# Performance work log

Hardware: AMD Instinct MI355X
Metric: run time of the kernel (lower is better)

Reference implementation:

```python
import jax, jax.numpy as jnp
import numpy as np

LATENT, U_DIM, NUM_PROD, NUM_INJ, FEAT_C = 128, 30, 20, 10, 128
WELL_IN = LATENT + U_DIM + FEAT_C  # 286
HID = 64
B = 16384


def setup_inputs() -> dict:
    key = jax.random.key(0)
    ks = jax.random.split(key, 12)
    s = lambda fan_in: 1.0 / np.sqrt(fan_in)
    return {
        "zt": jax.random.normal(ks[0], (B, LATENT), jnp.float32),
        "dt": 1,
        "ut": jax.random.normal(ks[1], (B, U_DIM), jnp.float32),
        "well_features": jax.random.normal(ks[2], (B, NUM_PROD, FEAT_C), jnp.float32),
        # StructuredODEFunc params: dz/dt = -(L L^T) z + Bm u
        "L": jax.random.normal(ks[3], (LATENT, LATENT), jnp.float32) * s(LATENT),
        "Bm": jax.random.normal(ks[4], (LATENT, U_DIM), jnp.float32) * s(U_DIM),
        # per-well MLP heads, stacked: [P, in, out]
        "W1": jax.random.uniform(ks[5], (NUM_PROD, WELL_IN, HID), jnp.float32, -s(WELL_IN), s(WELL_IN)),
        "b1": jax.random.uniform(ks[6], (NUM_PROD, HID), jnp.float32, -s(WELL_IN), s(WELL_IN)),
        "W2": jax.random.uniform(ks[7], (NUM_PROD, HID, 2), jnp.float32, -s(HID), s(HID)),
        "b2": jax.random.uniform(ks[8], (NUM_PROD, 2), jnp.float32, -s(HID), s(HID)),
        # injector head: Linear(latent+u_dim, num_inj)
        "Wi": jax.random.uniform(ks[9], (LATENT + U_DIM, NUM_INJ), jnp.float32, -s(LATENT + U_DIM), s(LATENT + U_DIM)),
        "bi": jax.random.uniform(ks[10], (NUM_INJ,), jnp.float32, -s(LATENT + U_DIM), s(LATENT + U_DIM)),
    }


def reference(zt, dt, ut, well_features, L, Bm, W1, b1, W2, b2, Wi, bi):
    # ODE step: A = -L L^T, f(z) = A z + Bm u; euler over t_span [0,1] -> one step h=1
    A = -(L @ L.T)                                  # [D, D]
    zt1 = zt + zt @ A.T + ut @ Bm.T                 # [B, D]
    zu = jnp.concatenate([zt1, ut], axis=-1)        # [B, D+U]
    # per-well heads, fused as batched gather-MLP
    zu_b = jnp.broadcast_to(zu[:, None, :], (zu.shape[0], NUM_PROD, zu.shape[1]))
    head_in = jnp.concatenate([zu_b, well_features], axis=-1)        # [B, P, WELL_IN]
    h = jax.nn.relu(jnp.einsum('bpi,pih->bph', head_in, W1) + b1)    # [B, P, 64]
    well_out = jnp.einsum('bph,pho->bpo', h, W2) + b2                # [B, P, 2]
    well_out = well_out.reshape(well_out.shape[0], NUM_PROD * 2)     # concat order matches loop
    inj_out = zu @ Wi + bi                                           # [B, num_inj]
    yt1 = jnp.concatenate([well_out, inj_out], axis=-1)              # [B, 2P+I]
    return zt1, yt1
```

## Files before the change

kernel.cpp:

```cpp
#include <hip/hip_runtime.h>

#define BATCH   16384
#define LATENT  128
#define U_DIM   30
#define NUM_PROD 20
#define NUM_INJ 10
#define FEAT_C  128
#define WELL_IN 286
#define HID     64
#define ZT1_N   (BATCH*LATENT)
#define OUT_ROW (NUM_PROD*2+NUM_INJ)

typedef unsigned short u16;
typedef __attribute__((ext_vector_type(8))) short  short8;
typedef __attribute__((ext_vector_type(4))) float  floatx4;

__device__ __forceinline__ u16 f2bf(float f){
    unsigned x = __builtin_bit_cast(unsigned, f);
    x += 0x7fffu + ((x >> 16) & 1u);
    return (u16)(x >> 16);
}
__device__ __forceinline__ short8 cvt8(floatx4 a, floatx4 b){
    short8 s;
    s[0]=(short)f2bf(a[0]); s[1]=(short)f2bf(a[1]);
    s[2]=(short)f2bf(a[2]); s[3]=(short)f2bf(a[3]);
    s[4]=(short)f2bf(b[0]); s[5]=(short)f2bf(b[1]);
    s[6]=(short)f2bf(b[2]); s[7]=(short)f2bf(b[3]);
    return s;
}

#define NW1  368640
#define NGS  20480
#define NWIS 2560
#define NW2S 20480
__device__ u16 g_w1s[NW1];
__device__ u16 g_gs [NGS];
__device__ u16 g_wis[NWIS];
__device__ u16 g_w2s[NW2S];

__global__ __launch_bounds__(256) void prep_kernel(
    const float* __restrict__ L, const float* __restrict__ Bm,
    const float* __restrict__ W1, const float* __restrict__ Wi,
    const float* __restrict__ W2)
{
    const int bx = blockIdx.x, t = threadIdx.x;
    if (bx < 180) {
        int s = bx*256 + t;
        int lane = s & 63;
        int rest = s >> 6;
        int kk = rest % 9, pn = rest / 9;
        int n0 = pn & 3, p = pn >> 2;
        int kbase = kk*32 + ((lane>>4)*8);
        int n = n0*16 + (lane & 15);
        short8 v;
#pragma unroll
        for (int j = 0; j < 8; j++) {
            int k = kbase + j;
            u16 b = 0;
            if (k < 158)        b = f2bf(W1[(p*WELL_IN + k)*HID + n]);
            else if (k >= 160)  b = f2bf(W1[(p*WELL_IN + (k-2))*HID + n]);
            v[j] = (short)b;
        }
        *(short8*)&g_w1s[(size_t)s*8] = v;
        return;
    }
    if (bx < 272) {
        int sid = (bx-180)*256 + t;
        if (sid < NW2S) {
            int j=sid&7, lane=(sid>>3)&63, rest=sid>>9;
            int kk=rest&1, p=rest>>1;
            int k=kk*32+((lane>>4)*8)+j, n=lane&15;
            g_w2s[sid] = (n<2) ? f2bf(W2[(p*HID+k)*2+n]) : (u16)0;
            return;
        }
        sid -= NW2S;
        if (sid < NWIS) {
            int j=sid&7, lane=(sid>>3)&63, kk=sid>>9;
            int k=kk*32+((lane>>4)*8)+j, n=lane&15;
            g_wis[sid] = (k<158 && n<NUM_INJ) ? f2bf(Wi[k*NUM_INJ+n]) : (u16)0;
            return;
        }
        sid -= NWIS;
        if (sid < 512) {
            int lane=sid&63, nt=sid>>6;
            int q=lane>>4, n=nt*16+(lane&15);
#pragma unroll
            for (int j = 0; j < 8; j++) {
                int u = q*8 + j;
                float v = (u < U_DIM) ? Bm[n*U_DIM + u] : 0.f;
                g_gs[((nt*5+4)*64 + lane)*8 + j] = f2bf(v);
            }
        }
        return;
    }
    const int mt = bx - 272;
    const int w = t>>6, lane=t&63, q=lane>>4, m=lane&15;
    floatx4 accG[2];
    accG[0]=(floatx4){0.f,0.f,0.f,0.f}; accG[1]=(floatx4){0.f,0.f,0.f,0.f};
#pragma unroll
    for (int kk = 0; kk < 4; kk++) {
        const float* ap = &L[(mt*16+m)*128 + kk*32 + q*8];
        short8 a = cvt8(*(const floatx4*)ap, *(const floatx4*)(ap+4));
#pragma unroll
        for (int ntl = 0; ntl < 2; ntl++) {
            int nt = w*2 + ntl;
            const float* bp = &L[(nt*16+m)*128 + kk*32 + q*8];
            short8 b = cvt8(*(const floatx4*)bp, *(const floatx4*)(bp+4));
            accG[ntl] = __builtin_amdgcn_mfma_f32_16x16x32_bf16(a, b, accG[ntl], 0, 0, 0);
        }
    }
#pragma unroll
    for (int ntl = 0; ntl < 2; ntl++)
#pragma unroll
        for (int r = 0; r < 4; r++) {
            int kg = mt*16 + q*4 + r;
            int n  = (w*2+ntl)*16 + m;
            float v = ((kg==n) ? 1.f : 0.f) - accG[ntl][r];
            int fi = ((n>>4)*5 + (kg>>5))*512 + (((kg>>3)&3)*16 + (n&15))*8 + (kg&7);
            g_gs[fi] = f2bf(v);
        }
}

__global__ __launch_bounds__(256) __attribute__((amdgpu_waves_per_eu(2,2)))
void ker_main(
    const float* __restrict__ zt, const float* __restrict__ ut,
    const float* __restrict__ wff, const float* __restrict__ b1,
    const float* __restrict__ b2,  const float* __restrict__ bi,
    const float* __restrict__ W2g,
    float* __restrict__ outf)
{
    __shared__ alignas(16) u16   zus[32][168];
    __shared__ alignas(16) float outs[32][50];
    const int t = threadIdx.x;
    const int row0 = blockIdx.x * 32;
    const int w = t >> 6, lane = t & 63, q = lane >> 4, m = lane & 15;

    floatx4 fr[16];
    auto issue = [&](int p){
#pragma unroll
        for (int rt = 0; rt < 2; rt++)
#pragma unroll
            for (int kk = 0; kk < 4; kk++) {
                const float* pb = &wff[((size_t)(row0 + rt*16 + m)*NUM_PROD + p)*FEAT_C + kk*32 + q*8];
                fr[rt*8 + kk*2 + 0] = *(const floatx4*)pb;
                fr[rt*8 + kk*2 + 1] = *(const floatx4*)(pb + 4);
            }
    };
    issue(w);

    for (int i = t; i < 1024; i += 256) {
        int r = i >> 5, c4 = i & 31;
        floatx4 v = *(const floatx4*)&zt[(size_t)(row0 + r)*128 + c4*4];
        u16* d = &zus[r][c4*4];
        d[0]=f2bf(v[0]); d[1]=f2bf(v[1]); d[2]=f2bf(v[2]); d[3]=f2bf(v[3]);
    }
    for (int i = t; i < 960; i += 256) {
        int r = i / U_DIM, c = i - r*U_DIM;
        zus[r][128 + c] = f2bf(ut[(row0 + r)*U_DIM + c]);
    }
    if (t < 64) zus[t >> 1][158 + (t & 1)] = 0;
    __syncthreads();

    {
        const int mt = w & 1, ng = (w >> 1) * 4;
        floatx4 acc[4];
#pragma unroll
        for (int c = 0; c < 4; c++) acc[c] = (floatx4){0.f,0.f,0.f,0.f};
#pragma unroll
        for (int kk = 0; kk < 5; kk++) {
            short8 a = *(const short8*)&zus[mt*16 + m][kk*32 + q*8];
#pragma unroll
            for (int c = 0; c < 4; c++) {
                short8 b = *(const short8*)&g_gs[(((ng+c)*5 + kk)*64 + lane)*8];
                acc[c] = __builtin_amdgcn_mfma_f32_16x16x32_bf16(a, b, acc[c], 0, 0, 0);
            }
        }
        __syncthreads();
#pragma unroll
        for (int c = 0; c < 4; c++)
#pragma unroll
            for (int r = 0; r < 4; r++) {
                int row = mt*16 + q*4 + r;
                int col = (ng+c)*16 + m;
                float v = acc[c][r];
                outf[(size_t)(row0 + row)*128 + col] = v;
                zus[row][col] = f2bf(v);
            }
    }
    __syncthreads();

    if (w == 3) {
        floatx4 ai[2];
        ai[0]=(floatx4){0.f,0.f,0.f,0.f}; ai[1]=(floatx4){0.f,0.f,0.f,0.f};
#pragma unroll
        for (int kk = 0; kk < 5; kk++) {
            short8 b = *(const short8*)&g_wis[(kk*64 + lane)*8];
#pragma unroll
            for (int rt = 0; rt < 2; rt++) {
                short8 a = *(const short8*)&zus[rt*16 + m][kk*32 + q*8];
                ai[rt] = __builtin_amdgcn_mfma_f32_16x16x32_bf16(a, b, ai[rt], 0, 0, 0);
            }
        }
        if (m < NUM_INJ) {
            float bv = bi[m];
#pragma unroll
            for (int rt = 0; rt < 2; rt++)
#pragma unroll
                for (int r = 0; r < 4; r++)
                    outs[rt*16 + q*4 + r][40 + m] = ai[rt][r] + bv;
        }
    }

    auto proc = [&](int p){
        short8 wa[2][4];
#pragma unroll
        for (int rt = 0; rt < 2; rt++)
#pragma unroll
            for (int kk = 0; kk < 4; kk++)
                wa[rt][kk] = cvt8(fr[rt*8 + kk*2], fr[rt*8 + kk*2 + 1]);
        if (p + 4 < NUM_PROD) issue(p + 4);

        floatx4 hacc[2][4];
#pragma unroll
        for (int rt = 0; rt < 2; rt++)
#pragma unroll
            for (int n0 = 0; n0 < 4; n0++) hacc[rt][n0] = (floatx4){0.f,0.f,0.f,0.f};
#pragma unroll
        for (int kk = 0; kk < 9; kk++) {
            short8 a0 = (kk < 5) ? *(const short8*)&zus[m][kk*32 + q*8]      : wa[0][kk-5];
            short8 a1 = (kk < 5) ? *(const short8*)&zus[16 + m][kk*32 + q*8] : wa[1][kk-5];
#pragma unroll
            for (int n0 = 0; n0 < 4; n0++) {
                short8 b = *(const short8*)&g_w1s[(((size_t)p*36 + n0*9 + kk)*64 + lane)*8];
                hacc[0][n0] = __builtin_amdgcn_mfma_f32_16x16x32_bf16(a0, b, hacc[0][n0], 0, 0, 0);
                hacc[1][n0] = __builtin_amdgcn_mfma_f32_16x16x32_bf16(a1, b, hacc[1][n0], 0, 0, 0);
            }
        }
        float bb[4], w2x[4], w2y[4];
#pragma unroll
        for (int n0 = 0; n0 < 4; n0++) {
            int col = n0*16 + m;
            bb[n0]  = b1[p*64 + col];
            w2x[n0] = W2g[(p*64 + col)*2 + 0];
            w2y[n0] = W2g[(p*64 + col)*2 + 1];
        }
        float bb2 = b2[p*2 + (m & 1)];
#pragma unroll
        for (int rt = 0; rt < 2; rt++) {
            float s[8];
#pragma unroll
            for (int r = 0; r < 4; r++) {
                float s0 = 0.f, s1 = 0.f;
#pragma unroll
                for (int n0 = 0; n0 < 4; n0++) {
                    float h = hacc[rt][n0][r] + bb[n0];
                    h = h > 0.f ? h : 0.f;
                    s0 += h * w2x[n0];
                    s1 += h * w2y[n0];
                }
                s[r*2+0] = s0; s[r*2+1] = s1;
            }
#pragma unroll
            for (int mask = 1; mask < 16; mask <<= 1)
#pragma unroll
                for (int i = 0; i < 8; i++)
                    s[i] += __shfl_xor(s[i], mask);
            float val = (m==0)?s[0]:(m==1)?s[1]:(m==2)?s[2]:(m==3)?s[3]
                       :(m==4)?s[4]:(m==5)?s[5]:(m==6)?s[6]:s[7];
            if (m < 8)
                outs[rt*16 + q*4 + (m>>1)][p*2 + (m&1)] = val + bb2;
        }
    };

    proc(w);
    proc(w + 4);
    proc(w + 8);
    proc(w + 12);
    proc(w + 16);
    __syncthreads();

    {
        const float* of = &outs[0][0];
        float* dst = outf + (size_t)ZT1_N + (size_t)row0 * OUT_ROW;
        for (int i = t; i < 400; i += 256)
            *(floatx4*)&dst[i*4] = *(const floatx4*)&of[i*4];
    }
}

extern "C" void kernel_launch(void* const* d_in, const int* in_sizes, int n_in,
                              void* d_out, int out_size, void* d_ws, size_t ws_size,
                              hipStream_t stream)
{
    const float* zt = (const float*)d_in[0];
    const float* ut = (const float*)d_in[2];
    const float* wf = (const float*)d_in[3];
    const float* L  = (const float*)d_in[4];
    const float* Bm = (const float*)d_in[5];
    const float* W1 = (const float*)d_in[6];
    const float* b1 = (const float*)d_in[7];
    const float* W2 = (const float*)d_in[8];
    const float* b2 = (const float*)d_in[9];
    const float* Wi = (const float*)d_in[10];
    const float* bi = (const float*)d_in[11];
    float* outf = (float*)d_out;

    prep_kernel<<<280, 256, 0, stream>>>(L, Bm, W1, Wi, W2);
    ker_main<<<BATCH/32, 256, 0, stream>>>(zt, ut, wf, b1, b2, bi, W2, outf);
}
```

Measured before the change: 295.9 us.

## Split each well's hidden dimension across waves with LDS-staged weights and features

Instead of each wave processing whole wells (5 wells per wave, all 64 hidden columns), all four waves now cooperate on every well. Each wave owns 16 hidden columns. The W1 slice and the converted well features are staged in LDS once per well, and partial second-layer sums are combined with LDS atomicAdd. W2, b1 and the b2-initialized output are preloaded into LDS, and the zu A-fragments are kept in registers. This cuts register pressure and redundant global loads, but adds two block barriers per well, LDS atomics, and only one well of feature prefetch ahead.

```diff
diff --git a/kernel.cpp b/kernel.cpp
--- a/kernel.cpp
+++ b/kernel.cpp
@@ -130,23 +130,28 @@
     float* __restrict__ outf)
 {
     __shared__ alignas(16) u16   zus[32][168];
+    __shared__ alignas(16) u16   wfb[4096];
+    __shared__ alignas(16) u16   w1l[18432];
     __shared__ alignas(16) float outs[32][50];
+    __shared__ alignas(16) float w2l[2560];
+    __shared__ alignas(16) float b1l[1280];
     const int t = threadIdx.x;
     const int row0 = blockIdx.x * 32;
     const int w = t >> 6, lane = t & 63, q = lane >> 4, m = lane & 15;
 
-    floatx4 fr[16];
+    const int lane_s = t & 63, cs = (t >> 6) & 3;
+    const int qs = lane_s >> 4, ms = lane_s & 15;
+
+    floatx4 fr[4];
     auto issue = [&](int p){
 #pragma unroll
-        for (int rt = 0; rt < 2; rt++)
-#pragma unroll
-            for (int kk = 0; kk < 4; kk++) {
-                const float* pb = &wff[((size_t)(row0 + rt*16 + m)*NUM_PROD + p)*FEAT_C + kk*32 + q*8];
-                fr[rt*8 + kk*2 + 0] = *(const floatx4*)pb;
-                fr[rt*8 + kk*2 + 1] = *(const floatx4*)(pb + 4);
-            }
+        for (int rt = 0; rt < 2; rt++) {
+            const float* pb = &wff[((size_t)(row0 + rt*16 + ms)*NUM_PROD + p)*FEAT_C + cs*32 + qs*8];
+            fr[rt*2+0] = *(const floatx4*)pb;
+            fr[rt*2+1] = *(const floatx4*)(pb + 4);
+        }
     };
-    issue(w);
+    issue(0);
 
     for (int i = t; i < 1024; i += 256) {
         int r = i >> 5, c4 = i & 31;
@@ -159,6 +164,12 @@
         zus[r][128 + c] = f2bf(ut[(row0 + r)*U_DIM + c]);
     }
     if (t < 64) zus[t >> 1][158 + (t & 1)] = 0;
+    for (int i = t; i < 2560; i += 256) w2l[i] = W2g[i];
+    for (int i = t; i < 1280; i += 256) b1l[i] = b1[i];
+    for (int i = t; i < 1600; i += 256) {
+        int col = i % 50;
+        (&outs[0][0])[i] = (col < 40) ? b2[col] : 0.f;
+    }
     __syncthreads();
 
     {
@@ -189,17 +200,21 @@
     }
     __syncthreads();
 
+    short8 za0[5], za1[5];
+#pragma unroll
+    for (int kk = 0; kk < 5; kk++) {
+        za0[kk] = *(const short8*)&zus[m][kk*32 + q*8];
+        za1[kk] = *(const short8*)&zus[16 + m][kk*32 + q*8];
+    }
+
     if (w == 3) {
         floatx4 ai[2];
         ai[0]=(floatx4){0.f,0.f,0.f,0.f}; ai[1]=(floatx4){0.f,0.f,0.f,0.f};
 #pragma unroll
         for (int kk = 0; kk < 5; kk++) {
             short8 b = *(const short8*)&g_wis[(kk*64 + lane)*8];
-#pragma unroll
-            for (int rt = 0; rt < 2; rt++) {
-                short8 a = *(const short8*)&zus[rt*16 + m][kk*32 + q*8];
-                ai[rt] = __builtin_amdgcn_mfma_f32_16x16x32_bf16(a, b, ai[rt], 0, 0, 0);
-            }
+            ai[0] = __builtin_amdgcn_mfma_f32_16x16x32_bf16(za0[kk], b, ai[0], 0, 0, 0);
+            ai[1] = __builtin_amdgcn_mfma_f32_16x16x32_bf16(za1[kk], b, ai[1], 0, 0, 0);
         }
         if (m < NUM_INJ) {
             float bv = bi[m];
@@ -211,54 +226,56 @@
         }
     }
 
-    auto proc = [&](int p){
+    for (int p = 0; p < NUM_PROD; p++) {
+        short8 wv[9];
+#pragma unroll
+        for (int i = 0; i < 9; i++) {
+            int f = (t >> 6) + i*4;
+            wv[i] = *(const short8*)&g_w1s[(((size_t)p*36 + f)*64 + lane_s)*8];
+        }
+        *(short8*)&wfb[((0*4 + cs)*64 + lane_s)*8] = cvt8(fr[0], fr[1]);
+        *(short8*)&wfb[((1*4 + cs)*64 + lane_s)*8] = cvt8(fr[2], fr[3]);
+#pragma unroll
+        for (int i = 0; i < 9; i++) {
+            int f = (t >> 6) + i*4;
+            *(short8*)&w1l[(size_t)(f*64 + lane_s)*8] = wv[i];
+        }
+        __syncthreads();
+        if (p + 1 < NUM_PROD) issue(p + 1);
+
+        short8 bq[9];
+#pragma unroll
+        for (int kk = 0; kk < 9; kk++)
+            bq[kk] = *(const short8*)&w1l[((w*9 + kk)*64 + lane)*8];
         short8 wa[2][4];
 #pragma unroll
         for (int rt = 0; rt < 2; rt++)
 #pragma unroll
             for (int kk = 0; kk < 4; kk++)
-                wa[rt][kk] = cvt8(fr[rt*8 + kk*2], fr[rt*8 + kk*2 + 1]);
-        if (p + 4 < NUM_PROD) issue(p + 4);
-
-        floatx4 hacc[2][4];
-#pragma unroll
-        for (int rt = 0; rt < 2; rt++)
-#pragma unroll
-            for (int n0 = 0; n0 < 4; n0++) hacc[rt][n0] = (floatx4){0.f,0.f,0.f,0.f};
+                wa[rt][kk] = *(const short8*)&wfb[((rt*4 + kk)*64 + lane)*8];
+        floatx4 h0 = (floatx4){0.f,0.f,0.f,0.f};
+        floatx4 h1 = (floatx4){0.f,0.f,0.f,0.f};
 #pragma unroll
         for (int kk = 0; kk < 9; kk++) {
-            short8 a0 = (kk < 5) ? *(const short8*)&zus[m][kk*32 + q*8]      : wa[0][kk-5];
-            short8 a1 = (kk < 5) ? *(const short8*)&zus[16 + m][kk*32 + q*8] : wa[1][kk-5];
-#pragma unroll
-            for (int n0 = 0; n0 < 4; n0++) {
-                short8 b = *(const short8*)&g_w1s[(((size_t)p*36 + n0*9 + kk)*64 + lane)*8];
-                hacc[0][n0] = __builtin_amdgcn_mfma_f32_16x16x32_bf16(a0, b, hacc[0][n0], 0, 0, 0);
-                hacc[1][n0] = __builtin_amdgcn_mfma_f32_16x16x32_bf16(a1, b, hacc[1][n0], 0, 0, 0);
-            }
-        }
-        float bb[4], w2x[4], w2y[4];
-#pragma unroll
-        for (int n0 = 0; n0 < 4; n0++) {
-            int col = n0*16 + m;
-            bb[n0]  = b1[p*64 + col];
-            w2x[n0] = W2g[(p*64 + col)*2 + 0];
-            w2y[n0] = W2g[(p*64 + col)*2 + 1];
-        }
-        float bb2 = b2[p*2 + (m & 1)];
+            short8 a0 = (kk < 5) ? za0[kk] : wa[0][kk-5];
+            short8 a1 = (kk < 5) ? za1[kk] : wa[1][kk-5];
+            h0 = __builtin_amdgcn_mfma_f32_16x16x32_bf16(a0, bq[kk], h0, 0, 0, 0);
+            h1 = __builtin_amdgcn_mfma_f32_16x16x32_bf16(a1, bq[kk], h1, 0, 0, 0);
+        }
+        const int col = w*16 + m;
+        const float bb  = b1l[p*64 + col];
+        const float w2x = w2l[(p*64 + col)*2 + 0];
+        const float w2y = w2l[(p*64 + col)*2 + 1];
 #pragma unroll
         for (int rt = 0; rt < 2; rt++) {
+            floatx4 hv = rt ? h1 : h0;
             float s[8];
 #pragma unroll
             for (int r = 0; r < 4; r++) {
-                float s0 = 0.f, s1 = 0.f;
-#pragma unroll
-                for (int n0 = 0; n0 < 4; n0++) {
-                    float h = hacc[rt][n0][r] + bb[n0];
-                    h = h > 0.f ? h : 0.f;
-                    s0 += h * w2x[n0];
-                    s1 += h * w2y[n0];
-                }
-                s[r*2+0] = s0; s[r*2+1] = s1;
+                float h = hv[r] + bb;
+                h = h > 0.f ? h : 0.f;
+                s[r*2+0] = h * w2x;
+                s[r*2+1] = h * w2y;
             }
 #pragma unroll
             for (int mask = 1; mask < 16; mask <<= 1)
@@ -268,16 +285,10 @@
             float val = (m==0)?s[0]:(m==1)?s[1]:(m==2)?s[2]:(m==3)?s[3]
                        :(m==4)?s[4]:(m==5)?s[5]:(m==6)?s[6]:s[7];
             if (m < 8)
-                outs[rt*16 + q*4 + (m>>1)][p*2 + (m&1)] = val + bb2;
-        }
-    };
-
-    proc(w);
-    proc(w + 4);
-    proc(w + 8);
-    proc(w + 12);
-    proc(w + 16);
-    __syncthreads();
+                atomicAdd(&outs[rt*16 + q*4 + (m>>1)][p*2 + (m&1)], val);
+        }
+        __syncthreads();
+    }
 
     {
         const float* of = &outs[0][0];
```

Result: no change. 293.0 us (-1.0%).
